# Performance work log

Hardware: AMD Instinct MI355X
Metric: run time of the kernel (lower is better)

The kernel has to match this reference:

```python
import jax, jax.numpy as jnp
import numpy as np

B, T, I, H, L = 32, 512, 256, 512, 4


def setup_inputs() -> dict:
    key = jax.random.key(0)
    ks = jax.random.split(key, 20)
    s = 0.01
    d = {"inputs": jax.random.normal(ks[0], (B, T, I), jnp.float32)}
    # layer-0 input->hidden weights (input dim I)
    for n, k in zip(["Wxi0", "Wxf0", "Wxo0", "Wxc0"], ks[1:5]):
        d[n] = jax.random.normal(k, (I, H), jnp.float32) * s
    # layers 1..L-1 input->hidden weights (input dim H), stacked
    for n, k in zip(["Wxi", "Wxf", "Wxo", "Wxc"], ks[5:9]):
        d[n] = jax.random.normal(k, (L - 1, H, H), jnp.float32) * s
    # hidden->hidden weights, stacked over layers
    for n, k in zip(["Whi", "Whf", "Who", "Whc"], ks[9:13]):
        d[n] = jax.random.normal(k, (L, H, H), jnp.float32) * s
    for n in ["bi", "bf", "bo", "bc"]:
        d[n] = jnp.zeros((L, H), jnp.float32)
    return d


def _lstm(inputs, Wxi0, Wxf0, Wxo0, Wxc0, Wxi, Wxf, Wxo, Wxc,
          Whi, Whf, Who, Whc, bi, bf, bo, bc):
    b, t, _ = inputs.shape
    h0 = jnp.zeros((L, b, H), inputs.dtype)
    c0 = jnp.zeros((L, b, H), inputs.dtype)

    def step(carry, x_t):
        h, c = carry  # each [L, B, H]
        new_h, new_c = [], []
        inp = x_t
        for l in range(L):
            if l == 0:
                wxi, wxf, wxo, wxc = Wxi0, Wxf0, Wxo0, Wxc0
            else:
                wxi, wxf, wxo, wxc = Wxi[l - 1], Wxf[l - 1], Wxo[l - 1], Wxc[l - 1]
            it = jax.nn.sigmoid(h[l] @ Whi[l] + inp @ wxi + bi[l])
            ft = jax.nn.sigmoid(h[l] @ Whf[l] + inp @ wxf + bf[l])
            ot = jax.nn.sigmoid(h[l] @ Who[l] + inp @ wxo + bo[l])
            ct_tilde = jnp.tanh(h[l] @ Whc[l] + inp @ wxc + bc[l])
            ct = ft * c[l] + it * ct_tilde
            ht = ot * jnp.tanh(ct)
            new_h.append(ht)
            new_c.append(ct)
            inp = ht
        return (jnp.stack(new_h), jnp.stack(new_c)), new_h[-1]

    _, outs = jax.lax.scan(step, (h0, c0), jnp.swapaxes(inputs, 0, 1))
    return jnp.swapaxes(outs, 0, 1)  # [B, T, H]


def reference(inputs, Wxi0, Wxf0, Wxo0, Wxc0, Wxi, Wxf, Wxo, Wxc,
              Whi, Whf, Who, Whc, bi, bf, bo, bc):
    return _lstm(inputs, Wxi0, Wxf0, Wxo0, Wxc0, Wxi, Wxf, Wxo, Wxc,
                 Whi, Whf, Who, Whc, bi, bf, bo, bc)
```

## Files before the change

kernel.cpp:

```cpp
#include <hip/hip_runtime.h>


constexpr int Bv = 32;
constexpr int Tv = 512;
constexpr int Iv = 256;
constexpr int Hv = 512;
constexpr int LAYv = 4;
constexpr int SLICES = 64;
constexpr int THREADS = 256;
constexpr int NKK = 32;
constexpr int WTAB = 2 * NKK * 64 * 8;
constexpr int SCR_STRIDE = 20;
constexpr unsigned SMEM_BYTES = WTAB * 2 * 2 + 4 * 16 * SCR_STRIDE * 4;

typedef short sfrag __attribute__((ext_vector_type(8)));
typedef short short4v __attribute__((ext_vector_type(4)));
typedef int   i32x2 __attribute__((ext_vector_type(2)));
typedef float facc  __attribute__((ext_vector_type(4)));
typedef float f32x4 __attribute__((ext_vector_type(4)));

struct Params {
  const float *x;
  const float *Wx0i, *Wx0f, *Wx0o, *Wx0c;
  const float *Wxi, *Wxf, *Wxo, *Wxc;
  const float *Whi, *Whf, *Who, *Whc;
  const float *bi, *bf, *bo, *bc;
  float *out;
  unsigned short *hbuf;
  unsigned char *flags;
  int dmask;
};

__device__ __forceinline__ unsigned short f2bf(float f) {
  unsigned int u = __builtin_bit_cast(unsigned int, f);
  u += 0x7FFFu + ((u >> 16) & 1u);
  return (unsigned short)(u >> 16);
}
__device__ __forceinline__ float bf2f(unsigned short s) {
  unsigned int u = ((unsigned int)s) << 16;
  return __builtin_bit_cast(float, u);
}

__device__ __forceinline__ int ld_flag_ushort_bypass(const unsigned char *p) {
  int v;
  asm volatile("global_load_ushort %0, %1, off sc0 sc1\n\t"
               "s_waitcnt vmcnt(0)"
               : "=v"(v) : "v"(p) : "memory");
  return v;
}
__device__ __forceinline__ void st_flagb_bypass(unsigned char *p) {
  asm volatile("global_store_byte %0, %1, off sc0 sc1" ::"v"(p), "v"(1)
               : "memory");
}
__device__ __forceinline__ void st_8b_bypass(unsigned short *p, i32x2 v) {
  asm volatile("global_store_dwordx2 %0, %1, off sc0 sc1" ::"v"(p), "v"(v)
               : "memory");
}
__device__ __forceinline__ void poll_line(const unsigned char *base) {
  while (ld_flag_ushort_bypass(base) != 0x0101) __builtin_amdgcn_s_sleep(1);
}

__global__ void __launch_bounds__(THREADS, 1) lstm_pipeline(Params p) {
  const int wg = blockIdx.x;
  const int l = wg >> 6;
  const int slice = wg & 63;
  const int tid = threadIdx.x;
  const int lane = tid & 63;
  const int w = tid >> 6;
  const int mt = w & 1;
  const int nt = w >> 1;

  extern __shared__ char smem[];
  unsigned short *wlds_hi = (unsigned short *)smem;
  unsigned short *wlds_lo = wlds_hi + WTAB;
  float *scratch = (float *)(smem + (size_t)WTAB * 2 * 2) +
                   (size_t)w * 16 * SCR_STRIDE;

  const float *Wh[4] = {p.Whi + (size_t)l * Hv * Hv, p.Whf + (size_t)l * Hv * Hv,
                        p.Who + (size_t)l * Hv * Hv, p.Whc + (size_t)l * Hv * Hv};
  const float *Wx[4];
  if (l == 0) { Wx[0] = p.Wx0i; Wx[1] = p.Wx0f; Wx[2] = p.Wx0o; Wx[3] = p.Wx0c; }
  else {
    size_t o = (size_t)(l - 1) * Hv * Hv;
    Wx[0] = p.Wxi + o; Wx[1] = p.Wxf + o; Wx[2] = p.Wxo + o; Wx[3] = p.Wxc + o;
  }
  const int kx_max = (l == 0) ? Iv : Hv;

  for (int idx = tid; idx < 2 * NKK * 64; idx += THREADS) {
    int lanei = idx & 63;
    int kk = (idx >> 6) & (NKK - 1);
    int nti = idx >> 11;
    int kbase = kk * 32 + (lanei >> 4) * 8;
    int n = nti * 16 + (lanei & 15);
    int jj = n >> 2, g = n & 3;
    int col = slice * 8 + jj;
    sfrag vh, vl;
#pragma unroll
    for (int j = 0; j < 8; ++j) {
      int k = kbase + j;
      float wv;
      if (k < Hv) wv = Wh[g][(size_t)k * Hv + col];
      else {
        int kx = k - Hv;
        wv = (kx < kx_max) ? Wx[g][(size_t)kx * Hv + col] : 0.f;
      }
      unsigned short h16 = f2bf(wv);
      vh[j] = (short)h16;
      vl[j] = (short)f2bf(wv - bf2f(h16));
    }
    *(sfrag *)&wlds_hi[(size_t)idx * 8] = vh;
    *(sfrag *)&wlds_lo[(size_t)idx * 8] = vl;
  }

  const int ubase = slice * 8 + nt * 4;
  f32x4 bi4 = *(const f32x4 *)&p.bi[l * Hv + ubase];
  f32x4 bf4 = *(const f32x4 *)&p.bf[l * Hv + ubase];
  f32x4 bo4 = *(const f32x4 *)&p.bo[l * Hv + ubase];
  f32x4 bc4 = *(const f32x4 *)&p.bc[l * Hv + ubase];
  float cst[4] = {0.f, 0.f, 0.f, 0.f};

  __syncthreads();

  const int m = mt * 16 + (lane & 15);
  const int kgrp = lane >> 4;
  unsigned char *flags = p.flags;
  unsigned short *hbuf = p.hbuf;
  const int dmask = p.dmask;

#define MFMA_BURST(A, KKB, CNT)                                                \
  {                                                                            \
    _Pragma("unroll") for (int j = 0; j < (CNT); ++j) {                        \
      sfrag bh =                                                               \
          *(const sfrag *)&wlds_hi[(size_t)((nt * NKK + (KKB) + j) * 64 + lane) * 8]; \
      sfrag bl =                                                               \
          *(const sfrag *)&wlds_lo[(size_t)((nt * NKK + (KKB) + j) * 64 + lane) * 8]; \
      acc0 = __builtin_amdgcn_mfma_f32_16x16x32_bf16(A[j], bh, acc0, 0, 0, 0); \
      acc1 = __builtin_amdgcn_mfma_f32_16x16x32_bf16(A[j], bl, acc1, 0, 0, 0); \
    }                                                                          \
  }

  for (int t = 0; t < Tv; ++t) {
    facc acc0 = {0.f, 0.f, 0.f, 0.f};
    facc acc1 = {0.f, 0.f, 0.f, 0.f};

    if (l == 0) {
      const float *xbp = p.x + ((size_t)m * Tv + t) * Iv + kgrp * 8;
#pragma unroll
      for (int kk = 0; kk < 8; ++kk) {
        f32x4 lo = *(const f32x4 *)(xbp + kk * 32);
        f32x4 hi = *(const f32x4 *)(xbp + kk * 32 + 4);
        sfrag ax;
#pragma unroll
        for (int j = 0; j < 4; ++j) {
          ax[j] = (short)f2bf(lo[j]);
          ax[4 + j] = (short)f2bf(hi[j]);
        }
        sfrag bh = *(const sfrag *)&wlds_hi[(size_t)((nt * NKK + 16 + kk) * 64 + lane) * 8];
        sfrag bl = *(const sfrag *)&wlds_lo[(size_t)((nt * NKK + 16 + kk) * 64 + lane) * 8];
        acc0 = __builtin_amdgcn_mfma_f32_16x16x32_bf16(ax, bh, acc0, 0, 0, 0);
        acc1 = __builtin_amdgcn_mfma_f32_16x16x32_bf16(ax, bl, acc1, 0, 0, 0);
      }
    } else {
      poll_line(flags + ((size_t)(t * LAYv + (l - 1)) * 2 + mt) * 128 + lane * 2);
      const unsigned short *hin =
          hbuf + ((size_t)(((t + 1) & dmask) * LAYv + (l - 1)) * Bv * Hv) +
          (size_t)m * Hv;
      sfrag ain[16];
#pragma unroll
      for (int kk = 0; kk < 16; ++kk)
        ain[kk] = *(const sfrag *)(hin + kk * 32 + kgrp * 8);
      MFMA_BURST(ain, 16, 16)
    }

    if (t > 0) {
      poll_line(flags + ((size_t)((t - 1) * LAYv + l) * 2 + mt) * 128 + lane * 2);
      const unsigned short *hrec =
          hbuf + ((size_t)((t & dmask) * LAYv + l) * Bv * Hv) + (size_t)m * Hv;
      sfrag arec[16];
#pragma unroll
      for (int kk = 0; kk < 16; ++kk)
        arec[kk] = *(const sfrag *)(hrec + kk * 32 + kgrp * 8);
      MFMA_BURST(arec, 0, 16)
    }

    {
      int rl = (lane >> 4) * 4;
      int cl = lane & 15;
#pragma unroll
      for (int r = 0; r < 4; ++r)
        scratch[(rl + r) * SCR_STRIDE + cl] = acc0[r] + acc1[r];
    }
    if (lane < 16) {
      int row = mt * 16 + lane;
      f32x4 q0 = *(const f32x4 *)&scratch[lane * SCR_STRIDE + 0];
      f32x4 q1 = *(const f32x4 *)&scratch[lane * SCR_STRIDE + 4];
      f32x4 q2 = *(const f32x4 *)&scratch[lane * SCR_STRIDE + 8];
      f32x4 q3 = *(const f32x4 *)&scratch[lane * SCR_STRIDE + 12];
      f32x4 qs[4] = {q0, q1, q2, q3};
      short4v sh;
      f32x4 ov;
#pragma unroll
      for (int u = 0; u < 4; ++u) {
        float pi = qs[u][0] + bi4[u];
        float pf = qs[u][1] + bf4[u];
        float po = qs[u][2] + bo4[u];
        float pc = qs[u][3] + bc4[u];
        float gi = 1.f / (1.f + __expf(-pi));
        float gf = 1.f / (1.f + __expf(-pf));
        float go = 1.f / (1.f + __expf(-po));
        float gc = tanhf(pc);
        cst[u] = gf * cst[u] + gi * gc;
        float hval = go * tanhf(cst[u]);
        sh[u] = (short)f2bf(hval);
        ov[u] = hval;
      }
      st_8b_bypass(&hbuf[((size_t)(((t + 1) & dmask) * LAYv + l) * Bv * Hv) +
                         (size_t)row * Hv + ubase],
                   __builtin_bit_cast(i32x2, sh));
      asm volatile("s_waitcnt vmcnt(0)" ::: "memory");
      if (lane == 0)
        st_flagb_bypass(flags + ((size_t)(t * LAYv + l) * 2 + mt) * 128 +
                        slice * 2 + nt);
      if (l == LAYv - 1)
        *(f32x4 *)&p.out[((size_t)row * Tv + t) * Hv + ubase] = ov;
    }
  }
#undef MFMA_BURST
}

extern "C" void kernel_launch(void *const *d_in, const int *in_sizes, int n_in,
                              void *d_out, int out_size, void *d_ws, size_t ws_size,
                              hipStream_t stream) {
  Params prm;
  prm.x = (const float *)d_in[0];
  prm.Wx0i = (const float *)d_in[1];
  prm.Wx0f = (const float *)d_in[2];
  prm.Wx0o = (const float *)d_in[3];
  prm.Wx0c = (const float *)d_in[4];
  prm.Wxi = (const float *)d_in[5];
  prm.Wxf = (const float *)d_in[6];
  prm.Wxo = (const float *)d_in[7];
  prm.Wxc = (const float *)d_in[8];
  prm.Whi = (const float *)d_in[9];
  prm.Whf = (const float *)d_in[10];
  prm.Who = (const float *)d_in[11];
  prm.Whc = (const float *)d_in[12];
  prm.bi = (const float *)d_in[13];
  prm.bf = (const float *)d_in[14];
  prm.bo = (const float *)d_in[15];
  prm.bc = (const float *)d_in[16];
  prm.out = (float *)d_out;

  size_t slot_bytes = (size_t)LAYv * Bv * Hv * sizeof(unsigned short);
  size_t fbytes = (size_t)Tv * LAYv * 2 * 128;
  size_t hslots = 512;
  if (ws_size < hslots * slot_bytes + fbytes) {
    hslots = 256;
    if (ws_size < hslots * slot_bytes + fbytes) return;
  }
  prm.dmask = (int)hslots - 1;
  prm.hbuf = (unsigned short *)d_ws;
  prm.flags = (unsigned char *)d_ws + hslots * slot_bytes;

  hipMemsetAsync(prm.flags, 0, fbytes, stream);

  hipFuncSetAttribute(reinterpret_cast<const void *>(lstm_pipeline),
                      hipFuncAttributeMaxDynamicSharedMemorySize, (int)SMEM_BYTES);

  hipLaunchKernelGGL(lstm_pipeline, dim3(LAYv * SLICES), dim3(THREADS),
                     SMEM_BYTES, stream, prm);
}
```

Baseline: 3.714 ms.

## Poll both dependency flags together, prefetch recurrent h, spread gate math across lanes

The two flag polls (previous layer and previous timestep) are merged into one loop that issues both loads before waiting. The recurrent h fragments are loaded before the input MFMA burst, so their latency overlaps with that compute. The gate nonlinearity is spread from 16 lanes handling 4 units each to all 64 lanes handling one unit each, with 2-byte bf16 stores replacing 8-byte stores. This shortens the serial tail on the recurrent critical path, at the cost of more, smaller global stores and waiting on both flags before any compute starts.

Result: slower. 7.554 ms (+103.4%).

```diff
diff --git a/kernel.cpp b/kernel.cpp
--- a/kernel.cpp
+++ b/kernel.cpp
@@ -14,8 +14,6 @@
 constexpr unsigned SMEM_BYTES = WTAB * 2 * 2 + 4 * 16 * SCR_STRIDE * 4;
 
 typedef short sfrag __attribute__((ext_vector_type(8)));
-typedef short short4v __attribute__((ext_vector_type(4)));
-typedef int   i32x2 __attribute__((ext_vector_type(2)));
 typedef float facc  __attribute__((ext_vector_type(4)));
 typedef float f32x4 __attribute__((ext_vector_type(4)));
 
@@ -41,23 +39,23 @@
   return __builtin_bit_cast(float, u);
 }
 
-__device__ __forceinline__ int ld_flag_ushort_bypass(const unsigned char *p) {
-  int v;
-  asm volatile("global_load_ushort %0, %1, off sc0 sc1\n\t"
+__device__ __forceinline__ void ld2_flag_bypass(const unsigned char *p0,
+                                                const unsigned char *p1,
+                                                int &a, int &b) {
+  asm volatile("global_load_ushort %0, %2, off sc0 sc1\n\t"
+               "global_load_ushort %1, %3, off sc0 sc1\n\t"
                "s_waitcnt vmcnt(0)"
-               : "=v"(v) : "v"(p) : "memory");
-  return v;
+               : "=&v"(a), "=&v"(b)
+               : "v"(p0), "v"(p1)
+               : "memory");
 }
 __device__ __forceinline__ void st_flagb_bypass(unsigned char *p) {
   asm volatile("global_store_byte %0, %1, off sc0 sc1" ::"v"(p), "v"(1)
                : "memory");
 }
-__device__ __forceinline__ void st_8b_bypass(unsigned short *p, i32x2 v) {
-  asm volatile("global_store_dwordx2 %0, %1, off sc0 sc1" ::"v"(p), "v"(v)
+__device__ __forceinline__ void st_short_bypass(unsigned short *p, unsigned short v) {
+  asm volatile("global_store_short %0, %1, off sc0 sc1" ::"v"(p), "v"(v)
                : "memory");
-}
-__device__ __forceinline__ void poll_line(const unsigned char *base) {
-  while (ld_flag_ushort_bypass(base) != 0x0101) __builtin_amdgcn_s_sleep(1);
 }
 
 __global__ void __launch_bounds__(THREADS, 1) lstm_pipeline(Params p) {
@@ -112,12 +110,16 @@
     *(sfrag *)&wlds_lo[(size_t)idx * 8] = vl;
   }
 
+  const int er = lane >> 2;
+  const int eu = lane & 3;
   const int ubase = slice * 8 + nt * 4;
-  f32x4 bi4 = *(const f32x4 *)&p.bi[l * Hv + ubase];
-  f32x4 bf4 = *(const f32x4 *)&p.bf[l * Hv + ubase];
-  f32x4 bo4 = *(const f32x4 *)&p.bo[l * Hv + ubase];
-  f32x4 bc4 = *(const f32x4 *)&p.bc[l * Hv + ubase];
-  float cst[4] = {0.f, 0.f, 0.f, 0.f};
+  const int ju = ubase + eu;
+  const int grow = mt * 16 + er;
+  const float bia_i = p.bi[l * Hv + ju];
+  const float bia_f = p.bf[l * Hv + ju];
+  const float bia_o = p.bo[l * Hv + ju];
+  const float bia_c = p.bc[l * Hv + ju];
+  float cst = 0.f;
 
   __syncthreads();
 
@@ -143,7 +145,42 @@
     facc acc0 = {0.f, 0.f, 0.f, 0.f};
     facc acc1 = {0.f, 0.f, 0.f, 0.f};
 
-    if (l == 0) {
+    if (t > 0 || l > 0) {
+      const unsigned char *fin =
+          (l > 0) ? flags + ((size_t)(t * LAYv + (l - 1)) * 2 + mt) * 128 + lane * 2
+                  : nullptr;
+      const unsigned char *frec =
+          (t > 0) ? flags + ((size_t)((t - 1) * LAYv + l) * 2 + mt) * 128 + lane * 2
+                  : nullptr;
+      const unsigned char *pa_ = fin ? fin : frec;
+      const unsigned char *pb_ = frec ? frec : fin;
+      int a, b;
+      ld2_flag_bypass(pa_, pb_, a, b);
+      while (a != 0x0101 || b != 0x0101) {
+        __builtin_amdgcn_s_sleep(1);
+        ld2_flag_bypass(pa_, pb_, a, b);
+      }
+    }
+
+    sfrag arec[16];
+    if (t > 0) {
+      const unsigned short *hrec =
+          hbuf + ((size_t)((t & dmask) * LAYv + l) * Bv * Hv) + (size_t)m * Hv;
+#pragma unroll
+      for (int kk = 0; kk < 16; ++kk)
+        arec[kk] = *(const sfrag *)(hrec + kk * 32 + kgrp * 8);
+    }
+
+    if (l > 0) {
+      const unsigned short *hin =
+          hbuf + ((size_t)(((t + 1) & dmask) * LAYv + (l - 1)) * Bv * Hv) +
+          (size_t)m * Hv;
+      sfrag ain[16];
+#pragma unroll
+      for (int kk = 0; kk < 16; ++kk)
+        ain[kk] = *(const sfrag *)(hin + kk * 32 + kgrp * 8);
+      MFMA_BURST(ain, 16, 16)
+    } else {
       const float *xbp = p.x + ((size_t)m * Tv + t) * Iv + kgrp * 8;
 #pragma unroll
       for (int kk = 0; kk < 8; ++kk) {
@@ -160,28 +197,9 @@
         acc0 = __builtin_amdgcn_mfma_f32_16x16x32_bf16(ax, bh, acc0, 0, 0, 0);
         acc1 = __builtin_amdgcn_mfma_f32_16x16x32_bf16(ax, bl, acc1, 0, 0, 0);
       }
-    } else {
-      poll_line(flags + ((size_t)(t * LAYv + (l - 1)) * 2 + mt) * 128 + lane * 2);
-      const unsigned short *hin =
-          hbuf + ((size_t)(((t + 1) & dmask) * LAYv + (l - 1)) * Bv * Hv) +
-          (size_t)m * Hv;
-      sfrag ain[16];
-#pragma unroll
-      for (int kk = 0; kk < 16; ++kk)
-        ain[kk] = *(const sfrag *)(hin + kk * 32 + kgrp * 8);
-      MFMA_BURST(ain, 16, 16)
-    }
-
-    if (t > 0) {
-      poll_line(flags + ((size_t)((t - 1) * LAYv + l) * 2 + mt) * 128 + lane * 2);
-      const unsigned short *hrec =
-          hbuf + ((size_t)((t & dmask) * LAYv + l) * Bv * Hv) + (size_t)m * Hv;
-      sfrag arec[16];
-#pragma unroll
-      for (int kk = 0; kk < 16; ++kk)
-        arec[kk] = *(const sfrag *)(hrec + kk * 32 + kgrp * 8);
-      MFMA_BURST(arec, 0, 16)
-    }
+    }
+
+    if (t > 0) { MFMA_BURST(arec, 0, 16) }
 
     {
       int rl = (lane >> 4) * 4;
@@ -190,40 +208,28 @@
       for (int r = 0; r < 4; ++r)
         scratch[(rl + r) * SCR_STRIDE + cl] = acc0[r] + acc1[r];
     }
-    if (lane < 16) {
-      int row = mt * 16 + lane;
-      f32x4 q0 = *(const f32x4 *)&scratch[lane * SCR_STRIDE + 0];
-      f32x4 q1 = *(const f32x4 *)&scratch[lane * SCR_STRIDE + 4];
-      f32x4 q2 = *(const f32x4 *)&scratch[lane * SCR_STRIDE + 8];
-      f32x4 q3 = *(const f32x4 *)&scratch[lane * SCR_STRIDE + 12];
-      f32x4 qs[4] = {q0, q1, q2, q3};
-      short4v sh;
-      f32x4 ov;
-#pragma unroll
-      for (int u = 0; u < 4; ++u) {
-        float pi = qs[u][0] + bi4[u];
-        float pf = qs[u][1] + bf4[u];
-        float po = qs[u][2] + bo4[u];
-        float pc = qs[u][3] + bc4[u];
-        float gi = 1.f / (1.f + __expf(-pi));
-        float gf = 1.f / (1.f + __expf(-pf));
-        float go = 1.f / (1.f + __expf(-po));
-        float gc = tanhf(pc);
-        cst[u] = gf * cst[u] + gi * gc;
-        float hval = go * tanhf(cst[u]);
-        sh[u] = (short)f2bf(hval);
-        ov[u] = hval;
-      }
-      st_8b_bypass(&hbuf[((size_t)(((t + 1) & dmask) * LAYv + l) * Bv * Hv) +
-                         (size_t)row * Hv + ubase],
-                   __builtin_bit_cast(i32x2, sh));
-      asm volatile("s_waitcnt vmcnt(0)" ::: "memory");
-      if (lane == 0)
-        st_flagb_bypass(flags + ((size_t)(t * LAYv + l) * 2 + mt) * 128 +
-                        slice * 2 + nt);
-      if (l == LAYv - 1)
-        *(f32x4 *)&p.out[((size_t)row * Tv + t) * Hv + ubase] = ov;
-    }
+    f32x4 q = *(const f32x4 *)&scratch[er * SCR_STRIDE + eu * 4];
+
+    float pi = q[0] + bia_i;
+    float pf = q[1] + bia_f;
+    float po = q[2] + bia_o;
+    float pc = q[3] + bia_c;
+    float gi = 1.f / (1.f + __expf(-pi));
+    float gf = 1.f / (1.f + __expf(-pf));
+    float go = 1.f / (1.f + __expf(-po));
+    float gc = tanhf(pc);
+    cst = gf * cst + gi * gc;
+    float hval = go * tanhf(cst);
+
+    st_short_bypass(&hbuf[((size_t)(((t + 1) & dmask) * LAYv + l) * Bv * Hv) +
+                          (size_t)grow * Hv + ju],
+                    f2bf(hval));
+    asm volatile("s_waitcnt vmcnt(0)" ::: "memory");
+    if (lane == 0)
+      st_flagb_bypass(flags + ((size_t)(t * LAYv + l) * 2 + mt) * 128 +
+                      slice * 2 + nt);
+    if (l == LAYv - 1)
+      p.out[((size_t)grow * Tv + t) * Hv + ju] = hval;
   }
 #undef MFMA_BURST
 }
```
